# Kernel tuning notes

Measured on AMD Instinct MI355X. Metric: run time of the kernel, lower is better.

The kernel has to match this reference:

```python
import jax, jax.numpy as jnp
import numpy as np

COST_CLASS = 1.0
COST_MASK = 1.0
COST_DICE = 1.0


def setup_inputs() -> dict:
    key = jax.random.key(0)
    k1, k2, k3, k4 = jax.random.split(key, 4)
    B, Q, T, H, W, C = 4, 100, 20, 128, 128, 80
    out_probs = jax.random.normal(k1, (B, Q, C), dtype=jnp.float32)
    out_masks = jax.random.uniform(k2, (B, Q, H, W), dtype=jnp.float32)
    target_masks = jax.random.uniform(k3, (B, T, H, W), dtype=jnp.float32)
    target_labels = jax.random.randint(k4, (B, T), 0, C, dtype=jnp.int64)
    return {"out_probs": out_probs, "out_masks": out_masks,
            "target_masks": target_masks, "target_labels": target_labels}


def reference(out_probs, out_masks, target_masks, target_labels):
    # out_probs: [B,Q,C]; out_masks: [B,Q,H,W]; target_masks: [B,T,H,W]; target_labels: [B,T]
    B, Q = out_probs.shape[:2]
    T = target_labels.shape[1]

    # Classification cost: -softmax(out_probs)[b, q, target_labels[b, t]] -> [B,Q,T]
    prob = jax.nn.softmax(out_probs, axis=-1)
    idx = jnp.broadcast_to(target_labels[:, None, :], (B, Q, T))
    cost_class = -jnp.take_along_axis(prob, idx, axis=2)

    out_flat = out_masks.reshape(B, Q, -1)      # [B,Q,HW]
    tgt_flat = target_masks.reshape(B, T, -1)   # [B,T,HW]

    # Pairwise L1 cost over pixels: [B,Q,T]
    cost_mask = jnp.abs(out_flat[:, :, None, :] - tgt_flat[:, None, :, :]).sum(-1)

    # Pairwise dice cost: numerator via batched matmul, sums broadcast.
    inter = jnp.einsum('bqn,btn->bqt', out_flat, tgt_flat)
    denom = out_flat.sum(-1)[:, :, None] + tgt_flat.sum(-1)[:, None, :]
    cost_dice = 1.0 - (2.0 * inter + 1.0) / (denom + 1.0)

    C_mat = COST_MASK * cost_mask + COST_CLASS * cost_class + COST_DICE * cost_dice
    return C_mat  # [B,Q,T] cost matrix (Hungarian assignment runs on CPU outside)
```

## Files before the change

### kernel.cpp

```cpp
#include <hip/hip_runtime.h>
#include <hip/hip_bf16.h>
#include <math.h>

#define B_ 4
#define Q_ 100
#define T_ 20
#define C_ 80
#define HW_ 16384

#define S_ 16
#define QG_ 4
#define GPB_ (Q_ / QG_)
#define GROUPS_ (B_ * GPB_)
#define SEG4_ (HW_ / S_ / 4)
#define TW_ 5
#define SUBS_ 4
#define QREC_ 41
#define REC_ (QG_ * QREC_ * SUBS_)
#define GWS_OFF ((size_t)GROUPS_ * S_ * REC_)

__device__ __forceinline__ float wave_reduce4(float v) {
    v += __shfl_down(v, 32);
    v += __shfl_down(v, 16);
    v += __shfl_down(v, 8);
    v += __shfl_down(v, 4);
    return v;
}

template <bool WITH_G>
__device__ __forceinline__ void partial_body(const float4* __restrict__ o4,
                                             const float4* __restrict__ g4,
                                             float* __restrict__ rec,
                                             float* __restrict__ grec,
                                             int lane, int wave) {
    const int t0 = wave * TW_;

    float accL[QG_][TW_];
    float accI[QG_][TW_];
    float osum[QG_];
    float gsum[TW_];
#pragma unroll
    for (int qi = 0; qi < QG_; ++qi) {
        osum[qi] = 0.f;
#pragma unroll
        for (int tj = 0; tj < TW_; ++tj) { accL[qi][tj] = 0.f; accI[qi][tj] = 0.f; }
    }
#pragma unroll
    for (int tj = 0; tj < TW_; ++tj) gsum[tj] = 0.f;

    for (int i = lane; i < SEG4_; i += 64) {
        float4 o[QG_];
#pragma unroll
        for (int qi = 0; qi < QG_; ++qi) {
            o[qi] = o4[(size_t)qi * (HW_ / 4) + i];
            osum[qi] += (o[qi].x + o[qi].y) + (o[qi].z + o[qi].w);
        }
#pragma unroll
        for (int tj = 0; tj < TW_; ++tj) {
            const float4 g = g4[(size_t)(t0 + tj) * (HW_ / 4) + i];
            if (WITH_G) gsum[tj] += (g.x + g.y) + (g.z + g.w);
#pragma unroll
            for (int qi = 0; qi < QG_; ++qi) {
                accL[qi][tj] += (fabsf(o[qi].x - g.x) + fabsf(o[qi].y - g.y)) +
                                (fabsf(o[qi].z - g.z) + fabsf(o[qi].w - g.w));
                accI[qi][tj] = fmaf(o[qi].x, g.x, accI[qi][tj]);
                accI[qi][tj] = fmaf(o[qi].y, g.y, accI[qi][tj]);
                accI[qi][tj] = fmaf(o[qi].z, g.z, accI[qi][tj]);
                accI[qi][tj] = fmaf(o[qi].w, g.w, accI[qi][tj]);
            }
        }
    }

#pragma unroll
    for (int qi = 0; qi < QG_; ++qi) {
#pragma unroll
        for (int tj = 0; tj < TW_; ++tj) {
            const float vL = wave_reduce4(accL[qi][tj]);
            const float vI = wave_reduce4(accI[qi][tj]);
            if (lane < SUBS_) {
                rec[(qi * QREC_ + (t0 + tj)) * SUBS_ + lane]      = vL;
                rec[(qi * QREC_ + 20 + (t0 + tj)) * SUBS_ + lane] = vI;
            }
        }
        const float vo = wave_reduce4(osum[qi]);
        if (wave == 0 && lane < SUBS_) rec[(qi * QREC_ + 40) * SUBS_ + lane] = vo;
    }
    if (WITH_G) {
#pragma unroll
        for (int tj = 0; tj < TW_; ++tj) {
            const float vg = wave_reduce4(gsum[tj]);
            if (lane < SUBS_) grec[(t0 + tj) * SUBS_ + lane] = vg;
        }
    }
}

__global__ __launch_bounds__(256) void partial_kernel(const float* __restrict__ outm,
                                                      const float* __restrict__ tgtm,
                                                      float* __restrict__ ws) {
    const int r = blockIdx.x & 7;
    const int m = blockIdx.x >> 3;
    const int b = r >> 1;
    const int l = m * 2 + (r & 1);
    const int grp_local = l >> 4;
    const int seg = l & (S_ - 1);
    const int qbase = grp_local * QG_;
    const int grp = b * GPB_ + grp_local;

    const int lane = threadIdx.x & 63;
    const int wave = threadIdx.x >> 6;

    const float4* o4 = (const float4*)(outm + ((size_t)b * Q_ + qbase) * HW_) + seg * SEG4_;
    const float4* g4 = (const float4*)(tgtm + (size_t)b * T_ * HW_) + seg * SEG4_;
    float* rec  = ws + (size_t)(grp * S_ + seg) * REC_;
    float* grec = ws + GWS_OFF + (size_t)(b * S_ + seg) * T_ * SUBS_;

    if (grp_local == 0) partial_body<true>(o4, g4, rec, grec, lane, wave);
    else                partial_body<false>(o4, g4, rec, grec, lane, wave);
}

__global__ __launch_bounds__(64) void finalize_kernel(const float* __restrict__ probs,
                                                      const int*   __restrict__ labels,
                                                      const float* __restrict__ ws,
                                                      float* __restrict__ out) {
    const int bq = blockIdx.x;
    const int b = bq / Q_;
    const int q = bq % Q_;
    const int grp = b * GPB_ + q / QG_;
    const int qi  = q % QG_;

    __shared__ float s_logit[C_];
    for (int c = threadIdx.x; c < C_; c += 64)
        s_logit[c] = probs[(size_t)bq * C_ + c];
    __syncthreads();

    const int t = threadIdx.x;
    if (t < T_) {
        float L = 0.f, I = 0.f, os = 0.f, ts = 0.f;
#pragma unroll
        for (int s = 0; s < S_; ++s) {
            const float4* r4 = (const float4*)(ws + (size_t)(grp * S_ + s) * REC_);
            const float4* d4 = (const float4*)(ws + GWS_OFF + (size_t)(b * S_ + s) * T_ * SUBS_);
            const float4 a = r4[qi * QREC_ + t];
            const float4 v = r4[qi * QREC_ + 20 + t];
            const float4 c = r4[qi * QREC_ + 40];
            const float4 d = d4[t];
            L  += (a.x + a.y) + (a.z + a.w);
            I  += (v.x + v.y) + (v.z + v.w);
            os += (c.x + c.y) + (c.z + c.w);
            ts += (d.x + d.y) + (d.z + d.w);
        }
        float mx = -INFINITY;
#pragma unroll
        for (int c = 0; c < C_; ++c) mx = fmaxf(mx, s_logit[c]);
        float sum = 0.f;
#pragma unroll
        for (int c = 0; c < C_; ++c) sum += __expf(s_logit[c] - mx);
        const int lab = labels[b * T_ + t];
        const float p = __expf(s_logit[lab] - mx) / sum;

        const float denom = os + ts;
        const float dice = 1.f - (2.f * I + 1.f) / (denom + 1.f);

        out[(size_t)bq * T_ + t] = L - p + dice;
    }
}

extern "C" void kernel_launch(void* const* d_in, const int* in_sizes, int n_in,
                              void* d_out, int out_size, void* d_ws, size_t ws_size,
                              hipStream_t stream) {
    const float* out_probs     = (const float*)d_in[0];
    const float* out_masks     = (const float*)d_in[1];
    const float* target_masks  = (const float*)d_in[2];
    const int*   target_labels = (const int*)d_in[3];
    float* out = (float*)d_out;

    float* partials = (float*)d_ws;

    partial_kernel<<<GROUPS_ * S_, 256, 0, stream>>>(out_masks, target_masks, partials);
    finalize_kernel<<<B_ * Q_, 64, 0, stream>>>(out_probs, target_labels, partials, out);
}
```

Before: 39.38 us.

## Retile partial kernel to two queries per block with eight pixel segments

The partial kernel now gives each block 2 queries instead of 4 and splits pixels into 8 segments instead of 16. The block count stays at 1600 while each block handles a longer pixel range. The pixel loop is fully unrolled and wave reductions now go to one lane, so the workspace holds one scalar per wave instead of 4 sub-partials. This cuts finalize-stage reads and register pressure. The cost is reloading the 20 target masks more often per query, since each target tile is now shared by only 2 queries.

```diff
diff --git a/kernel.cpp b/kernel.cpp
--- a/kernel.cpp
+++ b/kernel.cpp
@@ -8,88 +8,97 @@
 #define C_ 80
 #define HW_ 16384
 
-#define S_ 16
-#define QG_ 4
-#define GPB_ (Q_ / QG_)
-#define GROUPS_ (B_ * GPB_)
+#define S_ 8
+#define QP_ (Q_ / 2)
 #define SEG4_ (HW_ / S_ / 4)
+#define NIT_ (SEG4_ / 64)
 #define TW_ 5
-#define SUBS_ 4
-#define QREC_ 41
-#define REC_ (QG_ * QREC_ * SUBS_)
-#define GWS_OFF ((size_t)GROUPS_ * S_ * REC_)
 
-__device__ __forceinline__ float wave_reduce4(float v) {
+#define NBLK_ (B_ * QP_ * S_)
+#define WL_OFF 0
+#define WI_OFF (NBLK_ * 40)
+#define OS_OFF (WI_OFF + NBLK_ * 40)
+#define GS_OFF (OS_OFF + NBLK_ * 2)
+
+typedef float f32x4 __attribute__((ext_vector_type(4)));
+
+__device__ __forceinline__ float wred(float v) {
     v += __shfl_down(v, 32);
     v += __shfl_down(v, 16);
     v += __shfl_down(v, 8);
     v += __shfl_down(v, 4);
+    v += __shfl_down(v, 2);
+    v += __shfl_down(v, 1);
     return v;
 }
 
 template <bool WITH_G>
-__device__ __forceinline__ void partial_body(const float4* __restrict__ o4,
-                                             const float4* __restrict__ g4,
-                                             float* __restrict__ rec,
-                                             float* __restrict__ grec,
-                                             int lane, int wave) {
-    const int t0 = wave * TW_;
+__device__ __forceinline__ void partial_body(const f32x4* __restrict__ o4,
+                                             const f32x4* __restrict__ g4,
+                                             float* __restrict__ ws,
+                                             int blin, int b, int seg,
+                                             int lane, int ts) {
+    const int t0 = ts * TW_;
 
-    float accL[QG_][TW_];
-    float accI[QG_][TW_];
-    float osum[QG_];
-    float gsum[TW_];
+    float accL[2][TW_], accI[2][TW_], os[2], gs[TW_];
 #pragma unroll
-    for (int qi = 0; qi < QG_; ++qi) {
-        osum[qi] = 0.f;
+    for (int qi = 0; qi < 2; ++qi) {
+        os[qi] = 0.f;
 #pragma unroll
         for (int tj = 0; tj < TW_; ++tj) { accL[qi][tj] = 0.f; accI[qi][tj] = 0.f; }
     }
 #pragma unroll
-    for (int tj = 0; tj < TW_; ++tj) gsum[tj] = 0.f;
+    for (int tj = 0; tj < TW_; ++tj) gs[tj] = 0.f;
 
-    for (int i = lane; i < SEG4_; i += 64) {
-        float4 o[QG_];
 #pragma unroll
-        for (int qi = 0; qi < QG_; ++qi) {
-            o[qi] = o4[(size_t)qi * (HW_ / 4) + i];
-            osum[qi] += (o[qi].x + o[qi].y) + (o[qi].z + o[qi].w);
-        }
+    for (int it = 0; it < NIT_; ++it) {
+        const int ofs = it * 64;
+        const f32x4 o0 = o4[ofs];
+        const f32x4 o1 = o4[(HW_ / 4) + ofs];
+        os[0] += (o0.x + o0.y) + (o0.z + o0.w);
+        os[1] += (o1.x + o1.y) + (o1.z + o1.w);
 #pragma unroll
         for (int tj = 0; tj < TW_; ++tj) {
-            const float4 g = g4[(size_t)(t0 + tj) * (HW_ / 4) + i];
-            if (WITH_G) gsum[tj] += (g.x + g.y) + (g.z + g.w);
-#pragma unroll
-            for (int qi = 0; qi < QG_; ++qi) {
-                accL[qi][tj] += (fabsf(o[qi].x - g.x) + fabsf(o[qi].y - g.y)) +
-                                (fabsf(o[qi].z - g.z) + fabsf(o[qi].w - g.w));
-                accI[qi][tj] = fmaf(o[qi].x, g.x, accI[qi][tj]);
-                accI[qi][tj] = fmaf(o[qi].y, g.y, accI[qi][tj]);
-                accI[qi][tj] = fmaf(o[qi].z, g.z, accI[qi][tj]);
-                accI[qi][tj] = fmaf(o[qi].w, g.w, accI[qi][tj]);
-            }
+            const f32x4 g = g4[(size_t)(t0 + tj) * (HW_ / 4) + ofs];
+            if (WITH_G) gs[tj] += (g.x + g.y) + (g.z + g.w);
+            accL[0][tj] += (fabsf(o0.x - g.x) + fabsf(o0.y - g.y)) +
+                           (fabsf(o0.z - g.z) + fabsf(o0.w - g.w));
+            accI[0][tj] = fmaf(o0.x, g.x, accI[0][tj]);
+            accI[0][tj] = fmaf(o0.y, g.y, accI[0][tj]);
+            accI[0][tj] = fmaf(o0.z, g.z, accI[0][tj]);
+            accI[0][tj] = fmaf(o0.w, g.w, accI[0][tj]);
+            accL[1][tj] += (fabsf(o1.x - g.x) + fabsf(o1.y - g.y)) +
+                           (fabsf(o1.z - g.z) + fabsf(o1.w - g.w));
+            accI[1][tj] = fmaf(o1.x, g.x, accI[1][tj]);
+            accI[1][tj] = fmaf(o1.y, g.y, accI[1][tj]);
+            accI[1][tj] = fmaf(o1.z, g.z, accI[1][tj]);
+            accI[1][tj] = fmaf(o1.w, g.w, accI[1][tj]);
         }
     }
 
+    float* WL = ws + WL_OFF;
+    float* WI = ws + WI_OFF;
+    float* OS = ws + OS_OFF;
+    float* GS = ws + GS_OFF;
 #pragma unroll
-    for (int qi = 0; qi < QG_; ++qi) {
+    for (int qi = 0; qi < 2; ++qi) {
 #pragma unroll
         for (int tj = 0; tj < TW_; ++tj) {
-            const float vL = wave_reduce4(accL[qi][tj]);
-            const float vI = wave_reduce4(accI[qi][tj]);
-            if (lane < SUBS_) {
-                rec[(qi * QREC_ + (t0 + tj)) * SUBS_ + lane]      = vL;
-                rec[(qi * QREC_ + 20 + (t0 + tj)) * SUBS_ + lane] = vI;
+            const float vL = wred(accL[qi][tj]);
+            const float vI = wred(accI[qi][tj]);
+            if (lane == 0) {
+                WL[(blin * 4 + ts) * 10 + qi * TW_ + tj] = vL;
+                WI[(blin * 4 + ts) * 10 + qi * TW_ + tj] = vI;
             }
         }
-        const float vo = wave_reduce4(osum[qi]);
-        if (wave == 0 && lane < SUBS_) rec[(qi * QREC_ + 40) * SUBS_ + lane] = vo;
+        const float vo = wred(os[qi]);
+        if (ts == 0 && lane == 0) OS[blin * 2 + qi] = vo;
     }
     if (WITH_G) {
 #pragma unroll
         for (int tj = 0; tj < TW_; ++tj) {
-            const float vg = wave_reduce4(gsum[tj]);
-            if (lane < SUBS_) grec[(t0 + tj) * SUBS_ + lane] = vg;
+            const float vg = wred(gs[tj]);
+            if (lane == 0) GS[(b * S_ + seg) * T_ + t0 + tj] = vg;
         }
     }
 }
@@ -101,21 +110,18 @@
     const int m = blockIdx.x >> 3;
     const int b = r >> 1;
     const int l = m * 2 + (r & 1);
-    const int grp_local = l >> 4;
+    const int qp = l >> 3;
     const int seg = l & (S_ - 1);
-    const int qbase = grp_local * QG_;
-    const int grp = b * GPB_ + grp_local;
+    const int blin = (b * QP_ + qp) * S_ + seg;
 
     const int lane = threadIdx.x & 63;
-    const int wave = threadIdx.x >> 6;
+    const int ts   = threadIdx.x >> 6;
 
-    const float4* o4 = (const float4*)(outm + ((size_t)b * Q_ + qbase) * HW_) + seg * SEG4_;
-    const float4* g4 = (const float4*)(tgtm + (size_t)b * T_ * HW_) + seg * SEG4_;
-    float* rec  = ws + (size_t)(grp * S_ + seg) * REC_;
-    float* grec = ws + GWS_OFF + (size_t)(b * S_ + seg) * T_ * SUBS_;
+    const f32x4* o4 = (const f32x4*)(outm + ((size_t)b * Q_ + qp * 2) * HW_) + seg * SEG4_ + lane;
+    const f32x4* g4 = (const f32x4*)(tgtm + (size_t)b * T_ * HW_) + seg * SEG4_ + lane;
 
-    if (grp_local == 0) partial_body<true>(o4, g4, rec, grec, lane, wave);
-    else                partial_body<false>(o4, g4, rec, grec, lane, wave);
+    if (qp == 0) partial_body<true>(o4, g4, ws, blin, b, seg, lane, ts);
+    else         partial_body<false>(o4, g4, ws, blin, b, seg, lane, ts);
 }
 
 __global__ __launch_bounds__(64) void finalize_kernel(const float* __restrict__ probs,
@@ -125,29 +131,30 @@
     const int bq = blockIdx.x;
     const int b = bq / Q_;
     const int q = bq % Q_;
-    const int grp = b * GPB_ + q / QG_;
-    const int qi  = q % QG_;
+    const int qp = q >> 1;
+    const int qi = q & 1;
 
     __shared__ float s_logit[C_];
     for (int c = threadIdx.x; c < C_; c += 64)
         s_logit[c] = probs[(size_t)bq * C_ + c];
     __syncthreads();
 
+    const float* WL = ws + WL_OFF;
+    const float* WI = ws + WI_OFF;
+    const float* OS = ws + OS_OFF;
+    const float* GS = ws + GS_OFF;
+
     const int t = threadIdx.x;
     if (t < T_) {
-        float L = 0.f, I = 0.f, os = 0.f, ts = 0.f;
+        const int ts = t / TW_, tj = t % TW_;
+        float L = 0.f, I = 0.f, osum = 0.f, tsum = 0.f;
 #pragma unroll
-        for (int s = 0; s < S_; ++s) {
-            const float4* r4 = (const float4*)(ws + (size_t)(grp * S_ + s) * REC_);
-            const float4* d4 = (const float4*)(ws + GWS_OFF + (size_t)(b * S_ + s) * T_ * SUBS_);
-            const float4 a = r4[qi * QREC_ + t];
-            const float4 v = r4[qi * QREC_ + 20 + t];
-            const float4 c = r4[qi * QREC_ + 40];
-            const float4 d = d4[t];
-            L  += (a.x + a.y) + (a.z + a.w);
-            I  += (v.x + v.y) + (v.z + v.w);
-            os += (c.x + c.y) + (c.z + c.w);
-            ts += (d.x + d.y) + (d.z + d.w);
+        for (int seg = 0; seg < S_; ++seg) {
+            const int blin = (b * QP_ + qp) * S_ + seg;
+            L    += WL[(blin * 4 + ts) * 10 + qi * TW_ + tj];
+            I    += WI[(blin * 4 + ts) * 10 + qi * TW_ + tj];
+            osum += OS[blin * 2 + qi];
+            tsum += GS[(b * S_ + seg) * T_ + t];
         }
         float mx = -INFINITY;
 #pragma unroll
@@ -158,7 +165,7 @@
         const int lab = labels[b * T_ + t];
         const float p = __expf(s_logit[lab] - mx) / sum;
 
-        const float denom = os + ts;
+        const float denom = osum + tsum;
         const float dice = 1.f - (2.f * I + 1.f) / (denom + 1.f);
 
         out[(size_t)bq * T_ + t] = L - p + dice;
@@ -176,6 +183,6 @@
 
     float* partials = (float*)d_ws;
 
-    partial_kernel<<<GROUPS_ * S_, 256, 0, stream>>>(out_masks, target_masks, partials);
+    partial_kernel<<<B_ * QP_ * S_, 256, 0, stream>>>(out_masks, target_masks, partials);
     finalize_kernel<<<B_ * Q_, 64, 0, stream>>>(out_probs, target_labels, partials, out);
 }
```

Result: faster. 35.60 us (-9.6%).
